# Kernel optimization log

Measured on AMD Instinct MI355X. Metric: run time of the kernel, lower is better.

Reference implementation:

```python
import jax, jax.numpy as jnp
import numpy as np

EMBED = 1024
HEADS = 16
HEAD_DIM = EMBED // HEADS
OUT_DIM = 1024


def setup_inputs() -> dict:
    key = jax.random.key(0)
    ks = jax.random.split(key, 8)
    N, L = 2, 2048
    values = jax.random.normal(ks[0], (N, L, EMBED), dtype=jnp.float32)
    keys_t = jax.random.normal(ks[1], (N, L, EMBED), dtype=jnp.float32)
    query = jax.random.normal(ks[2], (N, L, EMBED), dtype=jnp.float32)
    s = 1.0 / np.sqrt(HEAD_DIM)
    Wv = jax.random.normal(ks[3], (HEAD_DIM, HEAD_DIM), dtype=jnp.float32) * s
    Wk = jax.random.normal(ks[4], (HEAD_DIM, HEAD_DIM), dtype=jnp.float32) * s
    Wq = jax.random.normal(ks[5], (HEAD_DIM, HEAD_DIM), dtype=jnp.float32) * s
    Wout = jax.random.normal(ks[6], (OUT_DIM, EMBED), dtype=jnp.float32) * (1.0 / np.sqrt(EMBED))
    bout = jax.random.normal(ks[7], (OUT_DIM,), dtype=jnp.float32) * 0.01
    return {"values": values, "keys": keys_t, "query": query,
            "Wv": Wv, "Wk": Wk, "Wq": Wq, "Wout": Wout, "bout": bout}


def reference(values, keys, query, Wv, Wk, Wq, Wout, bout):
    N, Lq, _ = query.shape
    Lk = keys.shape[1]
    # split into heads: (N, L, H, D)
    v = values.reshape(N, Lk, HEADS, HEAD_DIM)
    k = keys.reshape(N, Lk, HEADS, HEAD_DIM)
    q = query.reshape(N, Lq, HEADS, HEAD_DIM)
    # per-head shared linear projections (torch Linear: x @ W.T, no bias)
    v = jnp.einsum('nlhd,ed->nlhe', v, Wv)
    k = jnp.einsum('nlhd,ed->nlhe', k, Wk)
    q = jnp.einsum('nqhd,ed->nqhe', q, Wq)
    # scores (N, H, Q, K); NOTE: scale is 1/sqrt(embed_size), per original code
    scores = jnp.einsum('nqhd,nkhd->nhqk', q, k) / jnp.sqrt(jnp.float32(EMBED))
    attn = jax.nn.softmax(scores, axis=-1)
    out = jnp.einsum('nhqk,nkhd->nqhd', attn, v).reshape(N, Lq, EMBED)
    # fc_out: x @ Wout.T + bout
    return out @ Wout.T + bout
```

## Files before the change

kernel.cpp:

```cpp
#include <hip/hip_runtime.h>
#include <cstdint>

typedef __attribute__((ext_vector_type(8))) short short8;
typedef __attribute__((ext_vector_type(4))) float floatx4;
typedef __attribute__((ext_vector_type(4))) _Float16 half4;

#define DEV __device__ __forceinline__

constexpr int NB = 2, Lseq = 2048, NH = 16, HD = 64, EMB = 1024;
constexpr float QSCALE = 0.03125f * 1.4426950408889634f;

DEV uint16_t f2bf(float f) {
  uint32_t x = __builtin_bit_cast(uint32_t, f);
  x += 0x7fffu + ((x >> 16) & 1u);
  return (uint16_t)(x >> 16);
}

DEV uint32_t pack2(float lo, float hi) {
  uint32_t a = __builtin_bit_cast(uint32_t, lo) + 0x8000u;
  uint32_t b = __builtin_bit_cast(uint32_t, hi) + 0x8000u;
  return __builtin_amdgcn_perm(b, a, 0x07060302);
}

DEV uint32_t packh2(float lo, float hi) {
  return __builtin_bit_cast(uint32_t, __builtin_amdgcn_cvt_pkrtz(lo, hi));
}

DEV void gl_lds16(const void* g, void* l) {
  __builtin_amdgcn_global_load_lds((const __attribute__((address_space(1))) void*)g,
                                   (__attribute__((address_space(3))) void*)l, 16, 0, 0);
}

DEV short8 ld8bf(const float* p, float sc) {
  float4 u = *(const float4*)p;
  float4 v = *(const float4*)(p + 4);
  union { short8 s; uint32_t d[4]; } r;
  r.d[0] = pack2(u.x * sc, u.y * sc);
  r.d[1] = pack2(u.z * sc, u.w * sc);
  r.d[2] = pack2(v.x * sc, v.y * sc);
  r.d[3] = pack2(v.z * sc, v.w * sc);
  return r.s;
}

__global__ __launch_bounds__(256) void prep_kernel(
    const float* __restrict__ values, const float* __restrict__ keysrc,
    const float* __restrict__ query, const float* __restrict__ Wv,
    const float* __restrict__ Wk, const float* __restrict__ Wq,
    const float* __restrict__ Wout,
    uint16_t* __restrict__ qp, uint16_t* __restrict__ kp,
    uint16_t* __restrict__ vp, uint16_t* __restrict__ wbf) {
  const int t = threadIdx.x, w = t >> 6, lane = t & 63;
  const int quad = lane >> 4, l16 = lane & 15;
  const int wid = blockIdx.x * 4 + w;
  const int mat = wid >> 10, sub = wid & 1023;

  if (mat == 3) {
#pragma unroll
    for (int i = 0; i < 4; ++i) {
      int idx = sub * 256 + i * 64 + lane;
      float4 v = ((const float4*)Wout)[idx];
      uint2 p;
      p.x = pack2(v.x, v.y);
      p.y = pack2(v.z, v.w);
      ((uint2*)wbf)[idx] = p;
    }
    return;
  }

  floatx4 c[4][4];
#pragma unroll
  for (int i = 0; i < 4; ++i)
#pragma unroll
    for (int j = 0; j < 4; ++j) c[i][j] = floatx4{0.f, 0.f, 0.f, 0.f};

  if (mat < 2) {
    const float* src = mat ? keysrc : query;
    const float* W   = mat ? Wk : Wq;
    const float asc  = mat ? 1.f : QSCALE;
    uint16_t* dst    = mat ? kp : qp;
    const int R0 = sub * 64;
    short8 a[4][2], b[4][2];
#pragma unroll
    for (int dc = 0; dc < 2; ++dc) {
#pragma unroll
      for (int f = 0; f < 4; ++f) {
        a[f][dc] = ld8bf(W + (size_t)(f * 16 + l16) * 64 + dc * 32 + quad * 8, asc);
        b[f][dc] = ld8bf(src + (size_t)(R0 + f * 16 + l16) * 64 + dc * 32 + quad * 8, 1.f);
      }
    }
#pragma unroll
    for (int dc = 0; dc < 2; ++dc)
#pragma unroll
      for (int mf = 0; mf < 4; ++mf)
#pragma unroll
        for (int nf = 0; nf < 4; ++nf)
          c[mf][nf] = __builtin_amdgcn_mfma_f32_16x16x32_bf16(a[mf][dc], b[nf][dc], c[mf][nf], 0, 0, 0);
#pragma unroll
    for (int nf = 0; nf < 4; ++nf) {
      int r = R0 + nf * 16 + l16;
      int h = r & 15, l = (r >> 4) & 2047, n = r >> 15;
      uint16_t* drow = dst + ((size_t)(n * 16 + h) * 2048 + l) * 64;
#pragma unroll
      for (int mf = 0; mf < 4; ++mf) {
        uint2 pk;
        pk.x = pack2(c[mf][nf][0], c[mf][nf][1]);
        pk.y = pack2(c[mf][nf][2], c[mf][nf][3]);
        *(uint2*)(drow + mf * 16 + quad * 4) = pk;
      }
    }
  } else {
    const int nh = sub >> 5, L0 = (sub & 31) * 64;
    const int n = nh >> 4, h = nh & 15;
    short8 a[4][2], b[4][2];
#pragma unroll
    for (int dc = 0; dc < 2; ++dc) {
#pragma unroll
      for (int f = 0; f < 4; ++f) {
        a[f][dc] = ld8bf(values + (size_t)(n * 2048 + L0 + f * 16 + l16) * 1024 + h * 64 + dc * 32 + quad * 8, 1.f);
        b[f][dc] = ld8bf(Wv + (size_t)(f * 16 + l16) * 64 + dc * 32 + quad * 8, 1.f);
      }
    }
#pragma unroll
    for (int dc = 0; dc < 2; ++dc)
#pragma unroll
      for (int mf = 0; mf < 4; ++mf)
#pragma unroll
        for (int nf = 0; nf < 4; ++nf)
          c[mf][nf] = __builtin_amdgcn_mfma_f32_16x16x32_bf16(a[mf][dc], b[nf][dc], c[mf][nf], 0, 0, 0);
#pragma unroll
    for (int nf = 0; nf < 4; ++nf) {
      int d = nf * 16 + l16;
      uint16_t* drow = vp + ((size_t)nh * 64 + d) * 2048 + L0;
#pragma unroll
      for (int mf = 0; mf < 4; ++mf) {
        uint2 pk;
        pk.x = packh2(c[mf][nf][0], c[mf][nf][1]);
        pk.y = packh2(c[mf][nf][2], c[mf][nf][3]);
        *(uint2*)(drow + mf * 16 + quad * 4) = pk;
      }
    }
  }
}

__global__ __launch_bounds__(256, 4) void flash_kernel(const uint16_t* __restrict__ qp,
                                                       const uint16_t* __restrict__ kp,
                                                       const uint16_t* __restrict__ vp,
                                                       uint16_t* __restrict__ xg) {
  constexpr int kbn = 32;
  __shared__ uint16_t Kt[2][64 * 64];
  __shared__ uint16_t Vt[2][64 * 64];
  const int t = threadIdx.x;
  const int w = t >> 6, lane = t & 63, quad = lane >> 4, l16 = lane & 15;
  const int nh = blockIdx.x, qt = blockIdx.y;
  const int q0 = qt * 64 + w * 16;
  const uint16_t* Qb = qp + (size_t)nh * Lseq * HD;
  const uint16_t* Kb = kp + (size_t)nh * Lseq * HD;
  const uint16_t* Vb = vp + (size_t)nh * HD * Lseq;
  const int srow = lane >> 3, sc8 = (lane & 7) ^ (lane >> 3);

  short8 bq[2];
  bq[0] = *(const short8*)(Qb + (q0 + l16) * 64 + quad * 8);
  bq[1] = *(const short8*)(Qb + (q0 + l16) * 64 + 32 + quad * 8);

  floatx4 o[4];
  floatx4 lfr;
#pragma unroll
  for (int i = 0; i < 4; ++i) o[i] = floatx4{0.f, 0.f, 0.f, 0.f};
  lfr = floatx4{0.f, 0.f, 0.f, 0.f};
  const _Float16 one = (_Float16)1.0f;
  const half4 vone = {one, one, one, one};

#pragma unroll
  for (int i = 0; i < 2; ++i) {
    int r0 = w * 16 + i * 8;
    gl_lds16(Kb + (r0 + srow) * 64 + sc8 * 8, &Kt[0][r0 * 64]);
    gl_lds16(Vb + (size_t)(r0 + srow) * Lseq + sc8 * 8, &Vt[0][r0 * 64]);
  }

  for (int kb = 0; kb < kbn; ++kb) {
    __syncthreads();
    const int cur = kb & 1;
    if (kb + 1 < kbn) {
      const int nxt = cur ^ 1;
      const uint16_t* kg = Kb + (kb + 1) * (64 * 64);
#pragma unroll
      for (int i = 0; i < 2; ++i) {
        int r0 = w * 16 + i * 8;
        gl_lds16(kg + (r0 + srow) * 64 + sc8 * 8, &Kt[nxt][r0 * 64]);
        gl_lds16(Vb + (size_t)(r0 + srow) * Lseq + (kb + 1) * 64 + sc8 * 8, &Vt[nxt][r0 * 64]);
      }
    }

    floatx4 s[4];
#pragma unroll
    for (int kb16 = 0; kb16 < 4; ++kb16) s[kb16] = floatx4{0.f, 0.f, 0.f, 0.f};
#pragma unroll
    for (int dc = 0; dc < 2; ++dc) {
#pragma unroll
      for (int kb16 = 0; kb16 < 4; ++kb16) {
        int row = kb16 * 16 + l16;
        short8 ak = *(const short8*)(&Kt[cur][row * 64 + ((dc * 4 + quad) ^ (row & 7)) * 8]);
        s[kb16] = __builtin_amdgcn_mfma_f32_16x16x32_bf16(ak, bq[dc], s[kb16], 0, 0, 0);
      }
    }

    half4 bp[4];
#pragma unroll
    for (int kb16 = 0; kb16 < 4; ++kb16) {
      float p0 = __builtin_amdgcn_exp2f(s[kb16][0]);
      float p1 = __builtin_amdgcn_exp2f(s[kb16][1]);
      float p2 = __builtin_amdgcn_exp2f(s[kb16][2]);
      float p3 = __builtin_amdgcn_exp2f(s[kb16][3]);
      union { half4 h4; uint32_t d[2]; } u;
      u.d[0] = packh2(p0, p1);
      u.d[1] = packh2(p2, p3);
      bp[kb16] = u.h4;
    }
#pragma unroll
    for (int kb16 = 0; kb16 < 4; ++kb16)
      lfr = __builtin_amdgcn_mfma_f32_16x16x16f16(vone, bp[kb16], lfr, 0, 0, 0);

#pragma unroll
    for (int kb16 = 0; kb16 < 4; ++kb16) {
#pragma unroll
      for (int db = 0; db < 4; ++db) {
        int row = db * 16 + l16;
        int ch = (kb16 * 2 + (quad >> 1)) ^ (row & 7);
        half4 av = *(const half4*)(&Vt[cur][row * 64 + ch * 8 + (quad & 1) * 4]);
        o[db] = __builtin_amdgcn_mfma_f32_16x16x16f16(av, bp[kb16], o[db], 0, 0, 0);
      }
    }
  }

  const int nn = nh >> 4, h = nh & 15;
  const float inv = __builtin_amdgcn_rcpf(lfr[0]);
  uint16_t* xr = xg + ((size_t)(nn * 2048 + q0 + l16)) * 1024 + h * 64 + quad * 4;
#pragma unroll
  for (int db = 0; db < 4; ++db) {
    uint2 pk;
    pk.x = pack2(o[db][0] * inv, o[db][1] * inv);
    pk.y = pack2(o[db][2] * inv, o[db][3] * inv);
    *(uint2*)(xr + db * 16) = pk;
  }
}

__global__ __launch_bounds__(256, 2) void out_gemm(const uint16_t* __restrict__ Xg,
                                                   const uint16_t* __restrict__ Wb,
                                                   const float* __restrict__ bias,
                                                   float* __restrict__ out) {
  __shared__ uint16_t Xt[3][64 * 64];
  __shared__ uint16_t Wt[3][128 * 64];
  const int t = threadIdx.x, w = t >> 6, lane = t & 63, quad = lane >> 4, l16 = lane & 15;
  const int m0 = blockIdx.x * 64, o0 = blockIdx.y * 128;
  const int srow = lane >> 3, sc8 = (lane & 7) ^ (lane >> 3);

  floatx4 acc[8];
#pragma unroll
  for (int j = 0; j < 8; ++j) acc[j] = floatx4{0.f, 0.f, 0.f, 0.f};

  auto stage = [&](int buf, int kt) {
#pragma unroll
    for (int i = 0; i < 2; ++i) {
      int r0 = w * 16 + i * 8;
      gl_lds16(Xg + (size_t)(m0 + r0 + srow) * 1024 + kt * 64 + sc8 * 8, &Xt[buf][r0 * 64]);
    }
#pragma unroll
    for (int i = 0; i < 4; ++i) {
      int r0 = w * 32 + i * 8;
      gl_lds16(Wb + (size_t)(o0 + r0 + srow) * 1024 + kt * 64 + sc8 * 8, &Wt[buf][r0 * 64]);
    }
  };

  stage(0, 0);
  stage(1, 1);

  int cur = 0;
  for (int kt = 0; kt < 16; ++kt) {
    if (kt + 1 < 16) asm volatile("s_waitcnt vmcnt(6)" ::: "memory");
    else             asm volatile("s_waitcnt vmcnt(0)" ::: "memory");
    __builtin_amdgcn_s_barrier();
    if (kt + 2 < 16) {
      int tgt = cur + 2; if (tgt >= 3) tgt -= 3;
      stage(tgt, kt + 2);
    }
#pragma unroll
    for (int kc = 0; kc < 2; ++kc) {
      int ra = w * 16 + l16;
      short8 a = *(const short8*)(&Xt[cur][ra * 64 + ((kc * 4 + quad) ^ (ra & 7)) * 8]);
#pragma unroll
      for (int nf = 0; nf < 8; ++nf) {
        int rb = nf * 16 + l16;
        short8 b = *(const short8*)(&Wt[cur][rb * 64 + ((kc * 4 + quad) ^ (rb & 7)) * 8]);
        acc[nf] = __builtin_amdgcn_mfma_f32_16x16x32_bf16(a, b, acc[nf], 0, 0, 0);
      }
    }
    asm volatile("s_waitcnt lgkmcnt(0)" ::: "memory");
    cur = (cur + 1 == 3) ? 0 : cur + 1;
  }

#pragma unroll
  for (int nf = 0; nf < 8; ++nf) {
    float bv = bias[o0 + nf * 16 + l16];
#pragma unroll
    for (int r = 0; r < 4; ++r)
      out[(size_t)(m0 + w * 16 + quad * 4 + r) * 1024 + o0 + nf * 16 + l16] = acc[nf][r] + bv;
  }
}

extern "C" void kernel_launch(void* const* d_in, const int* in_sizes, int n_in,
                              void* d_out, int out_size, void* d_ws, size_t ws_size,
                              hipStream_t stream) {
  const float* values = (const float*)d_in[0];
  const float* keys   = (const float*)d_in[1];
  const float* query  = (const float*)d_in[2];
  const float* Wv     = (const float*)d_in[3];
  const float* Wk     = (const float*)d_in[4];
  const float* Wq     = (const float*)d_in[5];
  const float* Wout   = (const float*)d_in[6];
  const float* bout   = (const float*)d_in[7];
  float* out = (float*)d_out;
  (void)ws_size;

  uint16_t* ws  = (uint16_t*)d_ws;
  uint16_t* qp  = ws;
  uint16_t* kp  = ws + (size_t)4194304;
  uint16_t* vp  = ws + (size_t)8388608;
  uint16_t* wbf = ws + (size_t)12582912;
  uint16_t* xp  = ws + (size_t)13631488;

  prep_kernel<<<dim3(1024), dim3(256), 0, stream>>>(values, keys, query, Wv, Wk, Wq, Wout,
                                                    qp, kp, vp, wbf);
  flash_kernel<<<dim3(32, 32), dim3(256), 0, stream>>>(qp, kp, vp, xp);
  out_gemm<<<dim3(64, 8), dim3(256), 0, stream>>>(xp, wbf, bout, out);
}
```

Before: 176.5 us.

## Switch flash attention to 32x32 MFMA tiles with two waves per block

The attention kernel moves from 16x16 MFMA tiles to 32x32x16 MFMA instructions. Each wave now owns 32 query rows, and a block has 128 threads (2 waves) instead of 256. Probabilities are rearranged between lane halves with permlane32_swap so the score accumulator can feed the PV MFMA directly, and the LDS swizzle is changed to match the new access pattern. The goal is fewer MFMA issues and better operand reuse per instruction. In exchange there is higher register pressure and half as many waves per block for latency hiding.

```diff
diff --git a/kernel.cpp b/kernel.cpp
--- a/kernel.cpp
+++ b/kernel.cpp
@@ -3,18 +3,14 @@
 
 typedef __attribute__((ext_vector_type(8))) short short8;
 typedef __attribute__((ext_vector_type(4))) float floatx4;
+typedef __attribute__((ext_vector_type(16))) float floatx16;
 typedef __attribute__((ext_vector_type(4))) _Float16 half4;
+typedef __attribute__((ext_vector_type(8))) _Float16 half8;
 
 #define DEV __device__ __forceinline__
 
 constexpr int NB = 2, Lseq = 2048, NH = 16, HD = 64, EMB = 1024;
 constexpr float QSCALE = 0.03125f * 1.4426950408889634f;
-
-DEV uint16_t f2bf(float f) {
-  uint32_t x = __builtin_bit_cast(uint32_t, f);
-  x += 0x7fffu + ((x >> 16) & 1u);
-  return (uint16_t)(x >> 16);
-}
 
 DEV uint32_t pack2(float lo, float hi) {
   uint32_t a = __builtin_bit_cast(uint32_t, lo) + 0x8000u;
@@ -29,6 +25,13 @@
 DEV void gl_lds16(const void* g, void* l) {
   __builtin_amdgcn_global_load_lds((const __attribute__((address_space(1))) void*)g,
                                    (__attribute__((address_space(3))) void*)l, 16, 0, 0);
+}
+
+DEV void pl32(uint32_t& x, uint32_t& y) {
+  typedef __attribute__((ext_vector_type(2))) unsigned int uint2v;
+  uint2v r = __builtin_amdgcn_permlane32_swap(x, y, false, false);
+  x = r[0];
+  y = r[1];
 }
 
 DEV short8 ld8bf(const float* p, float sc) {
@@ -142,7 +145,7 @@
   }
 }
 
-__global__ __launch_bounds__(256, 4) void flash_kernel(const uint16_t* __restrict__ qp,
+__global__ __launch_bounds__(128, 2) void flash_kernel(const uint16_t* __restrict__ qp,
                                                        const uint16_t* __restrict__ kp,
                                                        const uint16_t* __restrict__ vp,
                                                        uint16_t* __restrict__ xg) {
@@ -150,98 +153,95 @@
   __shared__ uint16_t Kt[2][64 * 64];
   __shared__ uint16_t Vt[2][64 * 64];
   const int t = threadIdx.x;
-  const int w = t >> 6, lane = t & 63, quad = lane >> 4, l16 = lane & 15;
+  const int w = t >> 6, lane = t & 63, hi = lane >> 5, l32 = lane & 31;
   const int nh = blockIdx.x, qt = blockIdx.y;
-  const int q0 = qt * 64 + w * 16;
+  const int q0w = qt * 64 + w * 32;
   const uint16_t* Qb = qp + (size_t)nh * Lseq * HD;
   const uint16_t* Kb = kp + (size_t)nh * Lseq * HD;
   const uint16_t* Vb = vp + (size_t)nh * HD * Lseq;
   const int srow = lane >> 3, sc8 = (lane & 7) ^ (lane >> 3);
 
-  short8 bq[2];
-  bq[0] = *(const short8*)(Qb + (q0 + l16) * 64 + quad * 8);
-  bq[1] = *(const short8*)(Qb + (q0 + l16) * 64 + 32 + quad * 8);
-
-  floatx4 o[4];
-  floatx4 lfr;
-#pragma unroll
-  for (int i = 0; i < 4; ++i) o[i] = floatx4{0.f, 0.f, 0.f, 0.f};
-  lfr = floatx4{0.f, 0.f, 0.f, 0.f};
+  short8 bq[4];
+#pragma unroll
+  for (int dc = 0; dc < 4; ++dc)
+    bq[dc] = *(const short8*)(Qb + (size_t)(q0w + l32) * 64 + dc * 16 + hi * 8);
+
+  floatx16 o[2], lfr;
+#pragma unroll
+  for (int r = 0; r < 16; ++r) { o[0][r] = 0.f; o[1][r] = 0.f; lfr[r] = 0.f; }
   const _Float16 one = (_Float16)1.0f;
-  const half4 vone = {one, one, one, one};
-
-#pragma unroll
-  for (int i = 0; i < 2; ++i) {
-    int r0 = w * 16 + i * 8;
-    gl_lds16(Kb + (r0 + srow) * 64 + sc8 * 8, &Kt[0][r0 * 64]);
-    gl_lds16(Vb + (size_t)(r0 + srow) * Lseq + sc8 * 8, &Vt[0][r0 * 64]);
-  }
+  const half8 vones = {one, one, one, one, one, one, one, one};
+
+  auto stage = [&](int tile, int buf) {
+#pragma unroll
+    for (int i = 0; i < 4; ++i) {
+      int r0 = w * 32 + i * 8;
+      int sc = sc8 ^ i;
+      gl_lds16(Kb + (size_t)tile * 4096 + (r0 + srow) * 64 + sc * 8, &Kt[buf][r0 * 64]);
+      gl_lds16(Vb + (size_t)(r0 + srow) * Lseq + tile * 64 + sc * 8, &Vt[buf][r0 * 64]);
+    }
+  };
+
+  stage(0, 0);
 
   for (int kb = 0; kb < kbn; ++kb) {
     __syncthreads();
     const int cur = kb & 1;
-    if (kb + 1 < kbn) {
-      const int nxt = cur ^ 1;
-      const uint16_t* kg = Kb + (kb + 1) * (64 * 64);
-#pragma unroll
-      for (int i = 0; i < 2; ++i) {
-        int r0 = w * 16 + i * 8;
-        gl_lds16(kg + (r0 + srow) * 64 + sc8 * 8, &Kt[nxt][r0 * 64]);
-        gl_lds16(Vb + (size_t)(r0 + srow) * Lseq + (kb + 1) * 64 + sc8 * 8, &Vt[nxt][r0 * 64]);
-      }
-    }
-
-    floatx4 s[4];
-#pragma unroll
-    for (int kb16 = 0; kb16 < 4; ++kb16) s[kb16] = floatx4{0.f, 0.f, 0.f, 0.f};
-#pragma unroll
-    for (int dc = 0; dc < 2; ++dc) {
-#pragma unroll
-      for (int kb16 = 0; kb16 < 4; ++kb16) {
-        int row = kb16 * 16 + l16;
-        short8 ak = *(const short8*)(&Kt[cur][row * 64 + ((dc * 4 + quad) ^ (row & 7)) * 8]);
-        s[kb16] = __builtin_amdgcn_mfma_f32_16x16x32_bf16(ak, bq[dc], s[kb16], 0, 0, 0);
-      }
-    }
-
-    half4 bp[4];
-#pragma unroll
-    for (int kb16 = 0; kb16 < 4; ++kb16) {
-      float p0 = __builtin_amdgcn_exp2f(s[kb16][0]);
-      float p1 = __builtin_amdgcn_exp2f(s[kb16][1]);
-      float p2 = __builtin_amdgcn_exp2f(s[kb16][2]);
-      float p3 = __builtin_amdgcn_exp2f(s[kb16][3]);
-      union { half4 h4; uint32_t d[2]; } u;
-      u.d[0] = packh2(p0, p1);
-      u.d[1] = packh2(p2, p3);
-      bp[kb16] = u.h4;
-    }
-#pragma unroll
-    for (int kb16 = 0; kb16 < 4; ++kb16)
-      lfr = __builtin_amdgcn_mfma_f32_16x16x16f16(vone, bp[kb16], lfr, 0, 0, 0);
-
-#pragma unroll
-    for (int kb16 = 0; kb16 < 4; ++kb16) {
-#pragma unroll
-      for (int db = 0; db < 4; ++db) {
-        int row = db * 16 + l16;
-        int ch = (kb16 * 2 + (quad >> 1)) ^ (row & 7);
-        half4 av = *(const half4*)(&Vt[cur][row * 64 + ch * 8 + (quad & 1) * 4]);
-        o[db] = __builtin_amdgcn_mfma_f32_16x16x16f16(av, bp[kb16], o[db], 0, 0, 0);
+    if (kb + 1 < kbn) stage(kb + 1, cur ^ 1);
+
+#pragma unroll
+    for (int kt = 0; kt < 2; ++kt) {
+      floatx16 s;
+#pragma unroll
+      for (int r = 0; r < 16; ++r) s[r] = 0.f;
+      const int krow = kt * 32 + l32;
+      const int ksw = (krow & 7) ^ ((krow >> 3) & 3);
+#pragma unroll
+      for (int dc = 0; dc < 4; ++dc) {
+        short8 ak = *(const short8*)(&Kt[cur][krow * 64 + (((dc << 1) | hi) ^ ksw) * 8]);
+        s = __builtin_amdgcn_mfma_f32_32x32x16_bf16(ak, bq[dc], s, 0, 0, 0);
+      }
+      uint32_t a0 = packh2(__builtin_amdgcn_exp2f(s[0]), __builtin_amdgcn_exp2f(s[1]));
+      uint32_t a1 = packh2(__builtin_amdgcn_exp2f(s[2]), __builtin_amdgcn_exp2f(s[3]));
+      uint32_t b0 = packh2(__builtin_amdgcn_exp2f(s[4]), __builtin_amdgcn_exp2f(s[5]));
+      uint32_t b1 = packh2(__builtin_amdgcn_exp2f(s[6]), __builtin_amdgcn_exp2f(s[7]));
+      uint32_t c0 = packh2(__builtin_amdgcn_exp2f(s[8]), __builtin_amdgcn_exp2f(s[9]));
+      uint32_t c1 = packh2(__builtin_amdgcn_exp2f(s[10]), __builtin_amdgcn_exp2f(s[11]));
+      uint32_t d0 = packh2(__builtin_amdgcn_exp2f(s[12]), __builtin_amdgcn_exp2f(s[13]));
+      uint32_t d1 = packh2(__builtin_amdgcn_exp2f(s[14]), __builtin_amdgcn_exp2f(s[15]));
+      pl32(a0, b0); pl32(a1, b1); pl32(c0, d0); pl32(c1, d1);
+      union { half8 h; uint32_t u[4]; } f0, f1;
+      f0.u[0] = a0; f0.u[1] = a1; f0.u[2] = b0; f0.u[3] = b1;
+      f1.u[0] = c0; f1.u[1] = c1; f1.u[2] = d0; f1.u[3] = d1;
+
+      lfr = __builtin_amdgcn_mfma_f32_32x32x16_f16(vones, f0.h, lfr, 0, 0, 0);
+      lfr = __builtin_amdgcn_mfma_f32_32x32x16_f16(vones, f1.h, lfr, 0, 0, 0);
+
+#pragma unroll
+      for (int dt = 0; dt < 2; ++dt) {
+        const int vrow = dt * 32 + l32;
+        const int vsw = (vrow & 7) ^ ((vrow >> 3) & 3);
+        half8 av0 = *(const half8*)(&Vt[cur][vrow * 64 + ((kt * 4 + hi) ^ vsw) * 8]);
+        o[dt] = __builtin_amdgcn_mfma_f32_32x32x16_f16(av0, f0.h, o[dt], 0, 0, 0);
+        half8 av1 = *(const half8*)(&Vt[cur][vrow * 64 + ((kt * 4 + 2 + hi) ^ vsw) * 8]);
+        o[dt] = __builtin_amdgcn_mfma_f32_32x32x16_f16(av1, f1.h, o[dt], 0, 0, 0);
       }
     }
   }
 
   const int nn = nh >> 4, h = nh & 15;
   const float inv = __builtin_amdgcn_rcpf(lfr[0]);
-  uint16_t* xr = xg + ((size_t)(nn * 2048 + q0 + l16)) * 1024 + h * 64 + quad * 4;
-#pragma unroll
-  for (int db = 0; db < 4; ++db) {
-    uint2 pk;
-    pk.x = pack2(o[db][0] * inv, o[db][1] * inv);
-    pk.y = pack2(o[db][2] * inv, o[db][3] * inv);
-    *(uint2*)(xr + db * 16) = pk;
-  }
+  uint16_t* xr = xg + ((size_t)(nn * 2048 + q0w + l32)) * 1024 + h * 64;
+#pragma unroll
+  for (int dt = 0; dt < 2; ++dt)
+#pragma unroll
+    for (int rg = 0; rg < 4; ++rg) {
+      int dd = dt * 32 + rg * 8 + 4 * hi;
+      uint2 pk;
+      pk.x = pack2(o[dt][rg * 4] * inv, o[dt][rg * 4 + 1] * inv);
+      pk.y = pack2(o[dt][rg * 4 + 2] * inv, o[dt][rg * 4 + 3] * inv);
+      *(uint2*)(xr + dd) = pk;
+    }
 }
 
 __global__ __launch_bounds__(256, 2) void out_gemm(const uint16_t* __restrict__ Xg,
@@ -330,6 +330,6 @@
 
   prep_kernel<<<dim3(1024), dim3(256), 0, stream>>>(values, keys, query, Wv, Wk, Wq, Wout,
                                                     qp, kp, vp, wbf);
-  flash_kernel<<<dim3(32, 32), dim3(256), 0, stream>>>(qp, kp, vp, xp);
+  flash_kernel<<<dim3(32, 32), dim3(128), 0, stream>>>(qp, kp, vp, xp);
   out_gemm<<<dim3(64, 8), dim3(256), 0, stream>>>(xp, wbf, bout, out);
 }
```

After: 185.1 us. 1.05x slower.

## Stage projection outputs through LDS for coalesced stores and pad flash LDS tiles

Applied to the files above, without the earlier changes.

The prep kernel now writes its MFMA results into a per-wave swizzled LDS tile, then reads them back and stores full 16-byte rows to global memory. Before, each lane did scattered 8-byte stores into q/k/v. The flash kernel's K and V LDS tiles are split into 8-row groups with a padded stride of 528 elements, to reduce LDS bank conflicts when the MFMA operands are read. This adds 32KB of LDS to the prep kernel and a little extra address arithmetic in the flash inner loop. The unused f2bf helper is also removed.

```diff
diff --git a/kernel.cpp b/kernel.cpp
--- a/kernel.cpp
+++ b/kernel.cpp
@@ -9,12 +9,6 @@
 
 constexpr int NB = 2, Lseq = 2048, NH = 16, HD = 64, EMB = 1024;
 constexpr float QSCALE = 0.03125f * 1.4426950408889634f;
-
-DEV uint16_t f2bf(float f) {
-  uint32_t x = __builtin_bit_cast(uint32_t, f);
-  x += 0x7fffu + ((x >> 16) & 1u);
-  return (uint16_t)(x >> 16);
-}
 
 DEV uint32_t pack2(float lo, float hi) {
   uint32_t a = __builtin_bit_cast(uint32_t, lo) + 0x8000u;
@@ -49,6 +43,7 @@
     const float* __restrict__ Wout,
     uint16_t* __restrict__ qp, uint16_t* __restrict__ kp,
     uint16_t* __restrict__ vp, uint16_t* __restrict__ wbf) {
+  __shared__ uint16_t Tp[4][64 * 64];
   const int t = threadIdx.x, w = t >> 6, lane = t & 63;
   const int quad = lane >> 4, l16 = lane & 15;
   const int wid = blockIdx.x * 4 + w;
@@ -67,6 +62,7 @@
     return;
   }
 
+  uint16_t* T = Tp[w];
   floatx4 c[4][4];
 #pragma unroll
   for (int i = 0; i < 4; ++i)
@@ -95,18 +91,28 @@
 #pragma unroll
         for (int nf = 0; nf < 4; ++nf)
           c[mf][nf] = __builtin_amdgcn_mfma_f32_16x16x32_bf16(a[mf][dc], b[nf][dc], c[mf][nf], 0, 0, 0);
+
 #pragma unroll
     for (int nf = 0; nf < 4; ++nf) {
-      int r = R0 + nf * 16 + l16;
-      int h = r & 15, l = (r >> 4) & 2047, n = r >> 15;
-      uint16_t* drow = dst + ((size_t)(n * 16 + h) * 2048 + l) * 64;
+      int rl = nf * 16 + l16;
+      int swz = (rl & 7) ^ (((rl >> 3) & 1) << 2);
 #pragma unroll
       for (int mf = 0; mf < 4; ++mf) {
         uint2 pk;
         pk.x = pack2(c[mf][nf][0], c[mf][nf][1]);
         pk.y = pack2(c[mf][nf][2], c[mf][nf][3]);
-        *(uint2*)(drow + mf * 16 + quad * 4) = pk;
-      }
+        int s16 = (mf * 2 + (quad >> 1)) ^ swz;
+        *(uint2*)(&T[rl * 64 + s16 * 8 + (quad & 1) * 4]) = pk;
+      }
+    }
+#pragma unroll
+    for (int p = 0; p < 8; ++p) {
+      int rl2 = p * 8 + (lane >> 3), cch = lane & 7;
+      int swz = (rl2 & 7) ^ (((rl2 >> 3) & 1) << 2);
+      short8 vch = *(const short8*)(&T[rl2 * 64 + ((cch ^ swz) * 8)]);
+      int r = R0 + rl2;
+      int h = r & 15, l = (r >> 4) & 2047, n = r >> 15;
+      *(short8*)(dst + ((size_t)(n * 16 + h) * 2048 + l) * 64 + cch * 8) = vch;
     }
   } else {
     const int nh = sub >> 5, L0 = (sub & 31) * 64;
@@ -127,17 +133,26 @@
 #pragma unroll
         for (int nf = 0; nf < 4; ++nf)
           c[mf][nf] = __builtin_amdgcn_mfma_f32_16x16x32_bf16(a[mf][dc], b[nf][dc], c[mf][nf], 0, 0, 0);
+
 #pragma unroll
     for (int nf = 0; nf < 4; ++nf) {
       int d = nf * 16 + l16;
-      uint16_t* drow = vp + ((size_t)nh * 64 + d) * 2048 + L0;
+      int swz = (d & 7) ^ (((d >> 3) & 1) << 2);
 #pragma unroll
       for (int mf = 0; mf < 4; ++mf) {
         uint2 pk;
         pk.x = packh2(c[mf][nf][0], c[mf][nf][1]);
         pk.y = packh2(c[mf][nf][2], c[mf][nf][3]);
-        *(uint2*)(drow + mf * 16 + quad * 4) = pk;
-      }
+        int s16 = (mf * 2 + (quad >> 1)) ^ swz;
+        *(uint2*)(&T[d * 64 + s16 * 8 + (quad & 1) * 4]) = pk;
+      }
+    }
+#pragma unroll
+    for (int p = 0; p < 8; ++p) {
+      int d2 = p * 8 + (lane >> 3), cch = lane & 7;
+      int swz = (d2 & 7) ^ (((d2 >> 3) & 1) << 2);
+      short8 vch = *(const short8*)(&T[d2 * 64 + ((cch ^ swz) * 8)]);
+      *(short8*)(vp + ((size_t)nh * 64 + d2) * 2048 + L0 + cch * 8) = vch;
     }
   }
 }
@@ -147,8 +162,9 @@
                                                        const uint16_t* __restrict__ vp,
                                                        uint16_t* __restrict__ xg) {
   constexpr int kbn = 32;
-  __shared__ uint16_t Kt[2][64 * 64];
-  __shared__ uint16_t Vt[2][64 * 64];
+  constexpr int GS = 528;
+  __shared__ uint16_t Kt[2][8 * GS];
+  __shared__ uint16_t Vt[2][8 * GS];
   const int t = threadIdx.x;
   const int w = t >> 6, lane = t & 63, quad = lane >> 4, l16 = lane & 15;
   const int nh = blockIdx.x, qt = blockIdx.y;
@@ -173,8 +189,8 @@
 #pragma unroll
   for (int i = 0; i < 2; ++i) {
     int r0 = w * 16 + i * 8;
-    gl_lds16(Kb + (r0 + srow) * 64 + sc8 * 8, &Kt[0][r0 * 64]);
-    gl_lds16(Vb + (size_t)(r0 + srow) * Lseq + sc8 * 8, &Vt[0][r0 * 64]);
+    gl_lds16(Kb + (r0 + srow) * 64 + sc8 * 8, &Kt[0][(w * 2 + i) * GS]);
+    gl_lds16(Vb + (size_t)(r0 + srow) * Lseq + sc8 * 8, &Vt[0][(w * 2 + i) * GS]);
   }
 
   for (int kb = 0; kb < kbn; ++kb) {
@@ -186,8 +202,8 @@
 #pragma unroll
       for (int i = 0; i < 2; ++i) {
         int r0 = w * 16 + i * 8;
-        gl_lds16(kg + (r0 + srow) * 64 + sc8 * 8, &Kt[nxt][r0 * 64]);
-        gl_lds16(Vb + (size_t)(r0 + srow) * Lseq + (kb + 1) * 64 + sc8 * 8, &Vt[nxt][r0 * 64]);
+        gl_lds16(kg + (r0 + srow) * 64 + sc8 * 8, &Kt[nxt][(w * 2 + i) * GS]);
+        gl_lds16(Vb + (size_t)(r0 + srow) * Lseq + (kb + 1) * 64 + sc8 * 8, &Vt[nxt][(w * 2 + i) * GS]);
       }
     }
 
@@ -199,7 +215,9 @@
 #pragma unroll
       for (int kb16 = 0; kb16 < 4; ++kb16) {
         int row = kb16 * 16 + l16;
-        short8 ak = *(const short8*)(&Kt[cur][row * 64 + ((dc * 4 + quad) ^ (row & 7)) * 8]);
+        const uint16_t* ka = &Kt[cur][(row >> 3) * GS + (row & 7) * 64 +
+                                      (((dc * 4 + quad) ^ (row & 7)) * 8)];
+        short8 ak = *(const short8*)ka;
         s[kb16] = __builtin_amdgcn_mfma_f32_16x16x32_bf16(ak, bq[dc], s[kb16], 0, 0, 0);
       }
     }
@@ -226,7 +244,9 @@
       for (int db = 0; db < 4; ++db) {
         int row = db * 16 + l16;
         int ch = (kb16 * 2 + (quad >> 1)) ^ (row & 7);
-        half4 av = *(const half4*)(&Vt[cur][row * 64 + ch * 8 + (quad & 1) * 4]);
+        const uint16_t* va = &Vt[cur][(row >> 3) * GS + (row & 7) * 64 +
+                                      ch * 8 + (quad & 1) * 4];
+        half4 av = *(const half4*)va;
         o[db] = __builtin_amdgcn_mfma_f32_16x16x16f16(av, bp[kb16], o[db], 0, 0, 0);
       }
     }
```

Result: slower. 181.1 us (+2.6%).
